# Performance work log

Hardware: AMD Instinct MI355X
Metric: run time of the kernel (lower is better)

The kernel has to match this reference:

```python
import jax, jax.numpy as jnp
import numpy as np

N = 1024   # number of points (pairwise stage is N x N)
D = 16     # input_dim
H = 32     # hidden_dim
O = 3      # out_dim


def setup_inputs() -> dict:
    key = jax.random.key(0)
    ks = jax.random.split(key, 16)
    p = lambda k, shape: jax.random.normal(k, shape, jnp.float32) * 0.1
    return {
        'x': jax.random.normal(ks[0], (N, D), jnp.float32),
        'proj1_w': p(ks[1], (H, 2 * D)), 'proj1_b': p(ks[2], (H,)),
        'gru1_wih': p(ks[3], (3 * H, H)), 'gru1_whh': p(ks[4], (3 * H, H)),
        'gru1_bih': p(ks[5], (3 * H,)), 'gru1_bhh': p(ks[6], (3 * H,)),
        'proj2_w': p(ks[7], (H, 2 * H)), 'proj2_b': p(ks[8], (H,)),
        'gru2_wih': p(ks[9], (3 * H, H)), 'gru2_whh': p(ks[10], (3 * H, H)),
        'gru2_bih': p(ks[11], (3 * H,)), 'gru2_bhh': p(ks[12], (3 * H,)),
        'clf_w': p(ks[13], (O, H)), 'clf_b': p(ks[14], (O,)),
    }


def _pairwise_relu(feat, w, b):
    # feat: [N, F] -> relu(Linear(cat([f_i, f_j - f_i]))): [N, N, H]
    n, f = feat.shape
    fi = jnp.broadcast_to(feat[:, None, :], (n, n, f))
    fj = jnp.broadcast_to(feat[None, :, :], (n, n, f))
    diffs = jnp.concatenate([fi, fj - fi], axis=-1)  # [N, N, 2F]
    return jax.nn.relu(jnp.einsum('ijf,hf->ijh', diffs, w) + b)


def _gru_last(seq, wih, whh, bih, bhh):
    # seq: [B, T, H_in] (batch_first). Returns final hidden state [B, H].
    # PyTorch GRU gate order: r, z, n.
    xg = jnp.einsum('bti,gi->tbg', seq, wih) + bih  # precompute input gates [T,B,3H]
    h_dim = whh.shape[1]

    def step(h, g):
        xr, xz, xn = jnp.split(g, 3, axis=-1)
        hr, hz, hn = jnp.split(h @ whh.T + bhh, 3, axis=-1)
        r = jax.nn.sigmoid(xr + hr)
        z = jax.nn.sigmoid(xz + hz)
        n = jnp.tanh(xn + r * hn)
        return (1.0 - z) * n + z * h, None

    h0 = jnp.zeros((seq.shape[0], h_dim), seq.dtype)
    h_last, _ = jax.lax.scan(step, h0, xg)
    return h_last


def reference(x, proj1_w, proj1_b, gru1_wih, gru1_whh, gru1_bih, gru1_bhh,
              proj2_w, proj2_b, gru2_wih, gru2_whh, gru2_bih, gru2_bhh,
              clf_w, clf_b):
    out1 = _pairwise_relu(x, proj1_w, proj1_b)            # [N, N, H]
    h1 = _gru_last(out1, gru1_wih, gru1_whh, gru1_bih, gru1_bhh)  # [N, H]
    out2 = _pairwise_relu(h1, proj2_w, proj2_b)           # [N, N, H]
    h2 = _gru_last(out2, gru2_wih, gru2_whh, gru2_bih, gru2_bhh)  # [N, H]
    return h2 @ clf_w.T + clf_b                           # [N, O]
```

## Files before the change

### kernel.cpp

```cpp
#include <hip/hip_runtime.h>


typedef _Float16 hv2 __attribute__((ext_vector_type(2)));
typedef _Float16 hv8 __attribute__((ext_vector_type(8)));
typedef float    fv4 __attribute__((ext_vector_type(4)));
typedef unsigned uv4 __attribute__((ext_vector_type(4)));

__device__ __forceinline__ unsigned pkh(float a, float b) {
    auto t = __builtin_amdgcn_cvt_pkrtz(a, b);
    return __builtin_bit_cast(unsigned, t);
}
__device__ __forceinline__ fv4 splat4(float v) { return fv4{v, v, v, v}; }
#if __has_builtin(__builtin_amdgcn_rcpf)
__device__ __forceinline__ float frcp(float x) { return __builtin_amdgcn_rcpf(x); }
#else
__device__ __forceinline__ float frcp(float x) { return 1.f / x; }
#endif
#if __has_builtin(__builtin_amdgcn_exp2f)
__device__ __forceinline__ float fexp2(float x) { return __builtin_amdgcn_exp2f(x); }
#else
__device__ __forceinline__ float fexp2(float x) { return exp2f(x); }
#endif
#if __has_builtin(__builtin_amdgcn_fdot2)
__device__ __forceinline__ float d2(unsigned a, unsigned b, float c) {
    return __builtin_amdgcn_fdot2(__builtin_bit_cast(hv2, a),
                                  __builtin_bit_cast(hv2, b), c, false);
}
#else
__device__ __forceinline__ float d2(unsigned a, unsigned b, float c) {
    hv2 x = __builtin_bit_cast(hv2, a), y = __builtin_bit_cast(hv2, b);
    return fmaf((float)x.x, (float)y.x, fmaf((float)x.y, (float)y.y, c));
}
#endif
__device__ __forceinline__ float dpp_xor1(float x) {
    int r = __builtin_amdgcn_update_dpp(0, __builtin_bit_cast(int, x),
                                        0xB1, 0xF, 0xF, true);
    return __builtin_bit_cast(float, r);
}
__device__ __forceinline__ void half_swap(float x, float& lo_all, float& hi_all) {
    float d = x, s = x;
    asm("v_permlane32_swap_b32 %0, %1" : "+v"(d), "+v"(s));
    lo_all = d;
    hi_all = s;
}

#define SRZ (-1.44269504088896341f)
#define SN  ( 2.88539008177792682f)

__global__ void proj1_kernel(const float* __restrict__ x, const float* __restrict__ w,
                             const float* __restrict__ bias,
                             float* __restrict__ A, float* __restrict__ B) {
    int idx = blockIdx.x * 256 + threadIdx.x;
    int i = idx >> 5, h = idx & 31;
    float sa = bias[h];
    float sb = 0.f;
#pragma unroll
    for (int d = 0; d < 16; ++d) {
        float xv = x[i * 16 + d];
        float wa = w[h * 32 + d];
        float wb = w[h * 32 + 16 + d];
        sa += (wa - wb) * xv;
        sb += wb * xv;
    }
    A[i * 32 + h] = sa;
    B[i * 32 + h] = sb;
}

__global__ void proj2_kernel(const float* __restrict__ h1, const float* __restrict__ w,
                             const float* __restrict__ bias,
                             float* __restrict__ A, float* __restrict__ B) {
    int idx = blockIdx.x * 256 + threadIdx.x;
    int i = idx >> 5, h = idx & 31;
    float sa = bias[h];
    float sb = 0.f;
#pragma unroll
    for (int k = 0; k < 32; ++k) {
        float hv = h1[i * 32 + k];
        float wa = w[h * 64 + k];
        float wb = w[h * 64 + 32 + k];
        sa += (wa - wb) * hv;
        sb += wb * hv;
    }
    A[i * 32 + h] = sa;
    B[i * 32 + h] = sb;
}

__global__ __launch_bounds__(64, 1) void gru_kernel(
    const float* __restrict__ A, const float* __restrict__ B,
    const float* __restrict__ wih, const float* __restrict__ whh,
    const float* __restrict__ bih, const float* __restrict__ bhh,
    float* __restrict__ h_out,
    const float* __restrict__ clfw, const float* __restrict__ clfb,
    float* __restrict__ out3) {
    const int l = threadIdx.x;
    const int q = l >> 4;
    const int m0 = l & 15;
    const int m = l & 31;
    const int c = blockIdx.x;

    __shared__ float xg[6][16][20];

    hv8 WI[6];
#pragma unroll
    for (int T = 0; T < 6; ++T) {
        const float sc = (T < 4) ? SRZ : SN;
        int g = 16 * T + m0;
        uv4 wi;
#pragma unroll
        for (int r = 0; r < 4; ++r) {
            int lo = 4 * q + r;
            wi[r] = pkh(wih[g * 32 + lo] * sc, wih[g * 32 + lo + 16] * sc);
        }
        WI[T] = __builtin_bit_cast(hv8, wi);
    }
    float bi[6];
#pragma unroll
    for (int T = 0; T < 6; ++T) bi[T] = bih[16 * T + m0] * ((T < 4) ? SRZ : SN);

    const int grow = (l < 32) ? m : (32 + m);
    unsigned grz[16], wn2[16];
#pragma unroll
    for (int k = 0; k < 16; ++k) {
        grz[k] = pkh(whh[grow * 32 + 2 * k] * SRZ,     whh[grow * 32 + 2 * k + 1] * SRZ);
        wn2[k] = pkh(whh[(64 + m) * 32 + 2 * k] * SN,  whh[(64 + m) * 32 + 2 * k + 1] * SN);
    }
    const float brz  = bhh[grow] * SRZ;
    const float bhn2 = bhh[64 + m] * SN;

    const fv4* A4 = (const fv4*)A;
    const fv4* B4 = (const fv4*)B;
    const fv4 alo = A4[c * 8 + q];
    const fv4 ahi = A4[c * 8 + 4 + q];

    fv4 blo = B4[m0 * 8 + q], bhi = B4[m0 * 8 + 4 + q];

    float h_l = 0.f;

    const int Tq = m >> 4;
    const int mc = m & 15;
    const int TX = (l < 32) ? Tq : (2 + Tq);

    for (int c0 = 0; c0 < 1024; c0 += 16) {
        uv4 xb;
#pragma unroll
        for (int r = 0; r < 4; ++r)
            xb[r] = pkh(fmaxf(alo[r] + blo[r], 0.f), fmaxf(ahi[r] + bhi[r], 0.f));
        hv8 xf = __builtin_bit_cast(hv8, xb);

        int nc = (c0 + 16) & 1023;
        blo = B4[(nc + m0) * 8 + q];
        bhi = B4[(nc + m0) * 8 + 4 + q];

#pragma unroll
        for (int T = 0; T < 6; ++T) {
            fv4 D = __builtin_amdgcn_mfma_f32_16x16x32_f16(xf, WI[T], splat4(bi[T]), 0, 0, 0);
            fv4 e;
            if (T < 4) {
#pragma unroll
                for (int r = 0; r < 4; ++r) e[r] = fexp2(D[r]);
            } else {
                e = D;
            }
            *(fv4*)&xg[T][m0][4 * q] = e;
        }
        __syncthreads();

        fv4 Ex = *(const fv4*)&xg[TX][mc][0];
        fv4 Xn = *(const fv4*)&xg[4 + Tq][mc][0];

#pragma unroll
        for (int g = 0; g < 4; ++g) {
            const fv4 cEx = Ex, cXn = Xn;
            int ng = (g + 1) & 3;
            Ex = *(const fv4*)&xg[TX][mc][4 * ng];
            Xn = *(const fv4*)&xg[4 + Tq][mc][4 * ng];

#pragma unroll
            for (int j = 0; j < 4; ++j) {
                const float ex = cEx[j];
                const float xn = cXn[j];

                float hnb = dpp_xor1(h_l);
                hv2 hp;
                hp.x = (_Float16)h_l;
                hp.y = (_Float16)hnb;
                unsigned pk = __builtin_bit_cast(unsigned, hp);
                unsigned Hs[16];
#pragma unroll
                for (int k = 0; k < 16; ++k)
                    Hs[k] = (unsigned)__builtin_amdgcn_readlane((int)pk, 2 * k);

                float ga = brz, gb = 0.f, gc = 0.f, gd = 0.f;
#pragma unroll
                for (int k = 0; k < 4; ++k) {
                    ga = d2(grz[k],      Hs[k],      ga);
                    gb = d2(grz[k + 4],  Hs[k + 4],  gb);
                    gc = d2(grz[k + 8],  Hs[k + 8],  gc);
                    gd = d2(grz[k + 12], Hs[k + 12], gd);
                }
                float gfull = (ga + gb) + (gc + gd);
                float eh  = fexp2(gfull);
                float sig = frcp(fmaf(ex, eh, 1.f));

                float r, z;
                half_swap(sig, r, z);
                float omz = 1.f - z;
                float s   = fmaf(z, h_l, omz);
                float t2  = -2.f * omz;

                float na = bhn2, nb2 = 0.f, nc2 = 0.f, nd2 = 0.f;
#pragma unroll
                for (int k = 0; k < 4; ++k) {
                    na  = d2(wn2[k],      Hs[k],      na);
                    nb2 = d2(wn2[k + 4],  Hs[k + 4],  nb2);
                    nc2 = d2(wn2[k + 8],  Hs[k + 8],  nc2);
                    nd2 = d2(wn2[k + 12], Hs[k + 12], nd2);
                }
                float hn2 = (na + nb2) + (nc2 + nd2);

                float y  = fmaf(r, hn2, xn);
                float E  = fexp2(y);
                float rE = frcp(E + 1.f);
                h_l = fmaf(t2, rE, s);
            }
        }
        __syncthreads();
    }

    if (clfw) {
        float* hs = (float*)xg;
        if (l < 32) hs[m] = h_l;
        __syncthreads();
        if (l < 3) {
            float s = clfb[l];
#pragma unroll
            for (int k = 0; k < 32; ++k) s += clfw[l * 32 + k] * hs[k];
            out3[c * 3 + l] = s;
        }
    } else {
        if (l < 32) h_out[c * 32 + m] = h_l;
    }
}

extern "C" void kernel_launch(void* const* d_in, const int* in_sizes, int n_in,
                              void* d_out, int out_size, void* d_ws, size_t ws_size,
                              hipStream_t stream) {
    const float* x       = (const float*)d_in[0];
    const float* p1w     = (const float*)d_in[1];
    const float* p1b     = (const float*)d_in[2];
    const float* g1_wih  = (const float*)d_in[3];
    const float* g1_whh  = (const float*)d_in[4];
    const float* g1_bih  = (const float*)d_in[5];
    const float* g1_bhh  = (const float*)d_in[6];
    const float* p2w     = (const float*)d_in[7];
    const float* p2b     = (const float*)d_in[8];
    const float* g2_wih  = (const float*)d_in[9];
    const float* g2_whh  = (const float*)d_in[10];
    const float* g2_bih  = (const float*)d_in[11];
    const float* g2_bhh  = (const float*)d_in[12];
    const float* clfw    = (const float*)d_in[13];
    const float* clfb    = (const float*)d_in[14];

    float* ws = (float*)d_ws;
    float* A  = ws;
    float* Bt = ws + 32768;
    float* h  = ws + 65536;

    proj1_kernel<<<128, 256, 0, stream>>>(x, p1w, p1b, A, Bt);
    gru_kernel<<<1024, 64, 0, stream>>>(A, Bt, g1_wih, g1_whh, g1_bih, g1_bhh, h,
                                        nullptr, nullptr, nullptr);
    proj2_kernel<<<128, 256, 0, stream>>>(h, p2w, p2b, A, Bt);
    gru_kernel<<<1024, 64, 0, stream>>>(A, Bt, g2_wih, g2_whh, g2_bih, g2_bhh, h,
                                        clfw, clfb, (float*)d_out);
}
```

Measured before the change: 439.3 us.

## Double-buffer GRU input-gate chunks to overlap MFMA with serial recurrence

Splits the shared input-gate buffer into two halves. The MFMA computation for the next 16-step chunk is issued before the serial recurrence over the current chunk, so matrix work can interleave with the latency-bound scalar loop. This drops one barrier per chunk. The half_swap asm is also reworked to copy the value inside the asm with an early-clobber output, which gives the compiler a cleaner register allocation. The cost is doubled LDS use, longer unrolled code and more register pressure in a single-wave block.

New measurement: 447.2 us, median of 2. No clear change (+1.8%).

```diff
diff --git a/kernel.cpp b/kernel.cpp
--- a/kernel.cpp
+++ b/kernel.cpp
@@ -38,8 +38,10 @@
     return __builtin_bit_cast(float, r);
 }
 __device__ __forceinline__ void half_swap(float x, float& lo_all, float& hi_all) {
-    float d = x, s = x;
-    asm("v_permlane32_swap_b32 %0, %1" : "+v"(d), "+v"(s));
+    float d = x, s;
+    asm("v_mov_b32 %1, %0\n\t"
+        "v_permlane32_swap_b32 %0, %1"
+        : "+v"(d), "=&v"(s));
     lo_all = d;
     hi_all = s;
 }
@@ -84,6 +86,85 @@
     A[i * 32 + h] = sa;
     B[i * 32 + h] = sb;
 }
+
+#define CHUNK(BUF, TLOAD) do {                                                \
+    uv4 xb_;                                                                  \
+    _Pragma("unroll")                                                         \
+    for (int r_ = 0; r_ < 4; ++r_)                                            \
+        xb_[r_] = pkh(fmaxf(alo[r_] + blo[r_], 0.f),                          \
+                      fmaxf(ahi[r_] + bhi[r_], 0.f));                         \
+    hv8 xf_ = __builtin_bit_cast(hv8, xb_);                                   \
+    blo = B4[((TLOAD) + m0) * 8 + q];                                         \
+    bhi = B4[((TLOAD) + m0) * 8 + 4 + q];                                     \
+    _Pragma("unroll")                                                         \
+    for (int T_ = 0; T_ < 6; ++T_) {                                          \
+        fv4 D_ = __builtin_amdgcn_mfma_f32_16x16x32_f16(xf_, WI[T_],          \
+                                                splat4(bi[T_]), 0, 0, 0);     \
+        fv4 e_;                                                               \
+        if (T_ < 4) {                                                         \
+            _Pragma("unroll")                                                 \
+            for (int r_ = 0; r_ < 4; ++r_) e_[r_] = fexp2(D_[r_]);            \
+        } else {                                                              \
+            e_ = D_;                                                          \
+        }                                                                     \
+        *(fv4*)&xg[BUF][T_][m0][4 * q] = e_;                                  \
+    }                                                                         \
+} while (0)
+
+#define SERIAL16(BUF) do {                                                    \
+    fv4 Ex = *(const fv4*)&xg[BUF][TX][mc][0];                                \
+    fv4 Xn = *(const fv4*)&xg[BUF][4 + Tq][mc][0];                            \
+    _Pragma("unroll")                                                         \
+    for (int g_ = 0; g_ < 4; ++g_) {                                          \
+        const fv4 cEx = Ex, cXn = Xn;                                         \
+        int ng_ = (g_ + 1) & 3;                                               \
+        Ex = *(const fv4*)&xg[BUF][TX][mc][4 * ng_];                          \
+        Xn = *(const fv4*)&xg[BUF][4 + Tq][mc][4 * ng_];                      \
+        _Pragma("unroll")                                                     \
+        for (int j_ = 0; j_ < 4; ++j_) {                                      \
+            const float ex = cEx[j_];                                         \
+            const float xn = cXn[j_];                                         \
+            float hnb = dpp_xor1(h_l);                                        \
+            hv2 hp;                                                           \
+            hp.x = (_Float16)h_l;              \
+            hp.y = (_Float16)hnb;                                             \
+            unsigned pk = __builtin_bit_cast(unsigned, hp);                   \
+            unsigned Hs[16];                                                  \
+            _Pragma("unroll")                                                 \
+            for (int k_ = 0; k_ < 16; ++k_)                                   \
+                Hs[k_] = (unsigned)__builtin_amdgcn_readlane((int)pk, 2 * k_);\
+            float ga = brz, gb = 0.f, gc = 0.f, gd = 0.f;                     \
+            _Pragma("unroll")                                                 \
+            for (int k_ = 0; k_ < 4; ++k_) {                                  \
+                ga = d2(grz[k_],      Hs[k_],      ga);                       \
+                gb = d2(grz[k_ + 4],  Hs[k_ + 4],  gb);                       \
+                gc = d2(grz[k_ + 8],  Hs[k_ + 8],  gc);                       \
+                gd = d2(grz[k_ + 12], Hs[k_ + 12], gd);                       \
+            }                                                                 \
+            float gfull = (ga + gb) + (gc + gd);                              \
+            float eh  = fexp2(gfull);                                         \
+            float sig = frcp(fmaf(ex, eh, 1.f));                              \
+            float r, z;                                                       \
+            half_swap(sig, r, z);                                             \
+            float omz = 1.f - z;                                              \
+            float s   = fmaf(z, h_l, omz);                                    \
+            float t2  = -2.f * omz;                                           \
+            float na = bhn2, nb2 = 0.f, nc2 = 0.f, nd2 = 0.f;                 \
+            _Pragma("unroll")                                                 \
+            for (int k_ = 0; k_ < 4; ++k_) {                                  \
+                na  = d2(wn2[k_],      Hs[k_],      na);                      \
+                nb2 = d2(wn2[k_ + 4],  Hs[k_ + 4],  nb2);                     \
+                nc2 = d2(wn2[k_ + 8],  Hs[k_ + 8],  nc2);                     \
+                nd2 = d2(wn2[k_ + 12], Hs[k_ + 12], nd2);                     \
+            }                                                                 \
+            float hn2 = (na + nb2) + (nc2 + nd2);                             \
+            float y  = fmaf(r, hn2, xn);                                      \
+            float E  = fexp2(y);                                              \
+            float rE = frcp(E + 1.f);                                         \
+            h_l = fmaf(t2, rE, s);                                            \
+        }                                                                     \
+    }                                                                         \
+} while (0)
 
 __global__ __launch_bounds__(64, 1) void gru_kernel(
     const float* __restrict__ A, const float* __restrict__ B,
@@ -98,7 +179,7 @@
     const int m = l & 31;
     const int c = blockIdx.x;
 
-    __shared__ float xg[6][16][20];
+    __shared__ float xg[2][6][16][20];
 
     hv8 WI[6];
 #pragma unroll
@@ -140,92 +221,20 @@
     const int mc = m & 15;
     const int TX = (l < 32) ? Tq : (2 + Tq);
 
-    for (int c0 = 0; c0 < 1024; c0 += 16) {
-        uv4 xb;
-#pragma unroll
-        for (int r = 0; r < 4; ++r)
-            xb[r] = pkh(fmaxf(alo[r] + blo[r], 0.f), fmaxf(ahi[r] + bhi[r], 0.f));
-        hv8 xf = __builtin_bit_cast(hv8, xb);
-
-        int nc = (c0 + 16) & 1023;
-        blo = B4[(nc + m0) * 8 + q];
-        bhi = B4[(nc + m0) * 8 + 4 + q];
-
-#pragma unroll
-        for (int T = 0; T < 6; ++T) {
-            fv4 D = __builtin_amdgcn_mfma_f32_16x16x32_f16(xf, WI[T], splat4(bi[T]), 0, 0, 0);
-            fv4 e;
-            if (T < 4) {
-#pragma unroll
-                for (int r = 0; r < 4; ++r) e[r] = fexp2(D[r]);
-            } else {
-                e = D;
-            }
-            *(fv4*)&xg[T][m0][4 * q] = e;
-        }
+    CHUNK(0, 16);
+    __syncthreads();
+    for (int c0 = 0; c0 < 992; c0 += 32) {
+        CHUNK(1, (c0 + 32) & 1023);
+        SERIAL16(0);
         __syncthreads();
-
-        fv4 Ex = *(const fv4*)&xg[TX][mc][0];
-        fv4 Xn = *(const fv4*)&xg[4 + Tq][mc][0];
-
-#pragma unroll
-        for (int g = 0; g < 4; ++g) {
-            const fv4 cEx = Ex, cXn = Xn;
-            int ng = (g + 1) & 3;
-            Ex = *(const fv4*)&xg[TX][mc][4 * ng];
-            Xn = *(const fv4*)&xg[4 + Tq][mc][4 * ng];
-
-#pragma unroll
-            for (int j = 0; j < 4; ++j) {
-                const float ex = cEx[j];
-                const float xn = cXn[j];
-
-                float hnb = dpp_xor1(h_l);
-                hv2 hp;
-                hp.x = (_Float16)h_l;
-                hp.y = (_Float16)hnb;
-                unsigned pk = __builtin_bit_cast(unsigned, hp);
-                unsigned Hs[16];
-#pragma unroll
-                for (int k = 0; k < 16; ++k)
-                    Hs[k] = (unsigned)__builtin_amdgcn_readlane((int)pk, 2 * k);
-
-                float ga = brz, gb = 0.f, gc = 0.f, gd = 0.f;
-#pragma unroll
-                for (int k = 0; k < 4; ++k) {
-                    ga = d2(grz[k],      Hs[k],      ga);
-                    gb = d2(grz[k + 4],  Hs[k + 4],  gb);
-                    gc = d2(grz[k + 8],  Hs[k + 8],  gc);
-                    gd = d2(grz[k + 12], Hs[k + 12], gd);
-                }
-                float gfull = (ga + gb) + (gc + gd);
-                float eh  = fexp2(gfull);
-                float sig = frcp(fmaf(ex, eh, 1.f));
-
-                float r, z;
-                half_swap(sig, r, z);
-                float omz = 1.f - z;
-                float s   = fmaf(z, h_l, omz);
-                float t2  = -2.f * omz;
-
-                float na = bhn2, nb2 = 0.f, nc2 = 0.f, nd2 = 0.f;
-#pragma unroll
-                for (int k = 0; k < 4; ++k) {
-                    na  = d2(wn2[k],      Hs[k],      na);
-                    nb2 = d2(wn2[k + 4],  Hs[k + 4],  nb2);
-                    nc2 = d2(wn2[k + 8],  Hs[k + 8],  nc2);
-                    nd2 = d2(wn2[k + 12], Hs[k + 12], nd2);
-                }
-                float hn2 = (na + nb2) + (nc2 + nd2);
-
-                float y  = fmaf(r, hn2, xn);
-                float E  = fexp2(y);
-                float rE = frcp(E + 1.f);
-                h_l = fmaf(t2, rE, s);
-            }
-        }
+        CHUNK(0, (c0 + 48) & 1023);
+        SERIAL16(1);
         __syncthreads();
     }
+    CHUNK(1, 0);
+    SERIAL16(0);
+    __syncthreads();
+    SERIAL16(1);
 
     if (clfw) {
         float* hs = (float*)xg;
```
